# Kernel optimization log

Hardware: AMD Instinct MI355X
Metric: run time of the kernel (lower is better)

## Reference

```python
import jax, jax.numpy as jnp
import numpy as np

TOP_K = 2


def setup_inputs() -> dict:
    key = jax.random.key(0)
    k1, k2, k3 = jax.random.split(key, 3)
    inp = jax.random.normal(k1, (16384, 2048), dtype=jnp.float32)
    W = jax.random.normal(k2, (64, 2048), dtype=jnp.float32) * 0.02
    b = jax.random.normal(k3, (64,), dtype=jnp.float32) * 0.02
    return {"inp": inp, "W": W, "b": b}


def reference(inp, W, b):
    # gate logits: [tokens, num_expert]
    gate = jnp.einsum("td,ed->te", inp, W) + b
    # top-k over experts (lax.top_k returns sorted; torch used sorted=False,
    # so results match up to a per-token permutation of the k slots)
    top_val, top_idx = jax.lax.top_k(gate, TOP_K)  # [tokens, k]
    gate_score = jax.nn.softmax(top_val, axis=-1)[:, None, :]  # [tokens, 1, k]
    gate_top_k_idx = top_idx.reshape(-1)  # [tokens * k]
    return (gate_top_k_idx, gate_score)
```

## Files before the change

### kernel.cpp

```cpp
#include <hip/hip_runtime.h>
#include <math.h>


#define KDIM 2048
#define NEXP 64
#define TM 128
#define BK 32
#define LDSA 132
#define LDSW 68

__global__ __launch_bounds__(256) void gate_partial_kernel(
    const float* __restrict__ inp,
    const float* __restrict__ W,
    float* __restrict__ partial,
    int tokens, int kPerSplit)
{
    __shared__ float As[2][BK][LDSA];
    __shared__ float Ws[2][BK][LDSW];

    const int tid = threadIdx.x;
    const int tx  = tid & 7;
    const int ty  = tid >> 3;
    const int tokBase = blockIdx.x * TM;
    const int split   = blockIdx.y;
    const int k0      = split * kPerSplit;

    const int arow = tid >> 1;
    const int acol = (tid & 1) << 4;
    const int wrow = tid >> 2;
    const int wcol = (tid & 3) << 3;

    const float* aPtr = inp + (size_t)(tokBase + arow) * KDIM + k0 + acol;
    const float* wPtr = W   + (size_t)wrow * KDIM + k0 + wcol;

    float4 aReg[4], wReg[2];
    #pragma unroll
    for (int q = 0; q < 4; ++q) aReg[q] = *(const float4*)(aPtr + 4 * q);
    #pragma unroll
    for (int q = 0; q < 2; ++q) wReg[q] = *(const float4*)(wPtr + 4 * q);

    const int NT = kPerSplit / BK;

    #pragma unroll
    for (int q = 0; q < 4; ++q)
        #pragma unroll
        for (int j = 0; j < 4; ++j)
            As[0][acol + 4 * q + j][arow] = ((const float*)&aReg[q])[j];
    #pragma unroll
    for (int q = 0; q < 2; ++q)
        #pragma unroll
        for (int j = 0; j < 4; ++j)
            Ws[0][wcol + 4 * q + j][wrow] = ((const float*)&wReg[q])[j];

    if (NT > 1) {
        #pragma unroll
        for (int q = 0; q < 4; ++q) aReg[q] = *(const float4*)(aPtr + BK + 4 * q);
        #pragma unroll
        for (int q = 0; q < 2; ++q) wReg[q] = *(const float4*)(wPtr + BK + 4 * q);
    }
    __syncthreads();

    float acc[4][8];
    #pragma unroll
    for (int r = 0; r < 4; ++r)
        #pragma unroll
        for (int c = 0; c < 8; ++c) acc[r][c] = 0.0f;

    for (int kt = 0; kt < NT; ++kt) {
        const int cur = kt & 1;
        const int nxt = cur ^ 1;

        #pragma unroll 8
        for (int kk = 0; kk < BK; ++kk) {
            const float4 av  = *(const float4*)&As[cur][kk][ty << 2];
            const float4 wv0 = *(const float4*)&Ws[cur][kk][tx << 3];
            const float4 wv1 = *(const float4*)&Ws[cur][kk][(tx << 3) + 4];
            const float a[4] = {av.x, av.y, av.z, av.w};
            const float w[8] = {wv0.x, wv0.y, wv0.z, wv0.w,
                                wv1.x, wv1.y, wv1.z, wv1.w};
            #pragma unroll
            for (int r = 0; r < 4; ++r)
                #pragma unroll
                for (int c = 0; c < 8; ++c)
                    acc[r][c] = fmaf(a[r], w[c], acc[r][c]);
        }

        if (kt + 1 < NT) {
            #pragma unroll
            for (int q = 0; q < 4; ++q)
                #pragma unroll
                for (int j = 0; j < 4; ++j)
                    As[nxt][acol + 4 * q + j][arow] = ((const float*)&aReg[q])[j];
            #pragma unroll
            for (int q = 0; q < 2; ++q)
                #pragma unroll
                for (int j = 0; j < 4; ++j)
                    Ws[nxt][wcol + 4 * q + j][wrow] = ((const float*)&wReg[q])[j];
            if (kt + 2 < NT) {
                const int off = (kt + 2) * BK;
                #pragma unroll
                for (int q = 0; q < 4; ++q)
                    aReg[q] = *(const float4*)(aPtr + off + 4 * q);
                #pragma unroll
                for (int q = 0; q < 2; ++q)
                    wReg[q] = *(const float4*)(wPtr + off + 4 * q);
            }
        }
        __syncthreads();
    }

    const int eBase = tx << 3;
    #pragma unroll
    for (int r = 0; r < 4; ++r) {
        const int token = tokBase + (ty << 2) + r;
        float* p = &partial[((size_t)split * tokens + token) * NEXP + eBase];
        *(float4*)(p)     = make_float4(acc[r][0], acc[r][1], acc[r][2], acc[r][3]);
        *(float4*)(p + 4) = make_float4(acc[r][4], acc[r][5], acc[r][6], acc[r][7]);
    }
}

__global__ __launch_bounds__(256) void reduce_topk_kernel(
    const float* __restrict__ partial,
    const float* __restrict__ bias,
    float* __restrict__ out,
    int tokens, int S)
{
    const int tid = threadIdx.x;
    const int tx  = tid & 15;
    const int ty  = tid >> 4;
    const int token = blockIdx.x * 16 + ty;
    const int eBase = tx << 2;

    float4 v = make_float4(0.f, 0.f, 0.f, 0.f);
    for (int s = 0; s < S; ++s) {
        const float4 p = *(const float4*)&partial[((size_t)s * tokens + token) * NEXP + eBase];
        v.x += p.x; v.y += p.y; v.z += p.z; v.w += p.w;
    }
    const float4 bv = *(const float4*)&bias[eBase];
    float g[4] = { v.x + bv.x, v.y + bv.y, v.z + bv.z, v.w + bv.w };

    float v1 = g[0]; int i1 = eBase;
    float v2 = -INFINITY; int i2 = -1;
    #pragma unroll
    for (int c = 1; c < 4; ++c) {
        const float vv = g[c];
        const int   ii = eBase + c;
        if (vv > v1)      { v2 = v1; i2 = i1; v1 = vv; i1 = ii; }
        else if (vv > v2) { v2 = vv; i2 = ii; }
    }
    #pragma unroll
    for (int m = 1; m <= 8; m <<= 1) {
        const float ov1 = __shfl_xor(v1, m);
        const int   oi1 = __shfl_xor(i1, m);
        const float ov2 = __shfl_xor(v2, m);
        const int   oi2 = __shfl_xor(i2, m);
        const bool aw = (v1 > ov1) || (v1 == ov1 && i1 < oi1);
        const float nv1 = aw ? v1  : ov1;  const int ni1 = aw ? i1  : oi1;
        const float lv  = aw ? ov1 : v1;   const int li  = aw ? oi1 : i1;
        const float sv  = aw ? v2  : ov2;  const int si  = aw ? i2  : oi2;
        const bool sw = (sv > lv) || (sv == lv && si < li);
        v1 = nv1; i1 = ni1;
        v2 = sw ? sv : lv; i2 = sw ? si : li;
    }
    if (tx == 0) {
        const float e2 = expf(v2 - v1);
        const float denom = 1.0f + e2;
        out[2 * token]     = (float)i1;
        out[2 * token + 1] = (float)i2;
        out[tokens * 2 + 2 * token]     = 1.0f / denom;
        out[tokens * 2 + 2 * token + 1] = e2 / denom;
    }
}

extern "C" void kernel_launch(void* const* d_in, const int* in_sizes, int n_in,
                              void* d_out, int out_size, void* d_ws, size_t ws_size,
                              hipStream_t stream) {
    const float* inp  = (const float*)d_in[0];
    const float* W    = (const float*)d_in[1];
    const float* bias = (const float*)d_in[2];
    float* out = (float*)d_out;
    float* partial = (float*)d_ws;

    const int tokens = in_sizes[0] / KDIM;

    int S = 4;
    while (S > 1 && (size_t)S * tokens * NEXP * sizeof(float) > ws_size) S >>= 1;
    const int kPerSplit = KDIM / S;

    dim3 grid(tokens / TM, S);
    gate_partial_kernel<<<grid, 256, 0, stream>>>(inp, W, partial, tokens, kPerSplit);
    reduce_topk_kernel<<<tokens / 16, 256, 0, stream>>>(partial, bias, out, tokens, S);
}
```

Before: 214.8 us.

## Fuse split-K reduction and top-k into GEMM via last-block atomic counter

```diff
diff --git a/kernel.cpp b/kernel.cpp
--- a/kernel.cpp
+++ b/kernel.cpp
@@ -9,14 +9,18 @@
 #define LDSA 132
 #define LDSW 68
 
-__global__ __launch_bounds__(256) void gate_partial_kernel(
+__global__ __launch_bounds__(256) void gate_fused_kernel(
     const float* __restrict__ inp,
     const float* __restrict__ W,
+    const float* __restrict__ bias,
     float* __restrict__ partial,
-    int tokens, int kPerSplit)
+    int* __restrict__ ctr,
+    float* __restrict__ out,
+    int tokens, int kPerSplit, int S)
 {
     __shared__ float As[2][BK][LDSA];
     __shared__ float Ws[2][BK][LDSW];
+    __shared__ int lastFlag;
 
     const int tid = threadIdx.x;
     const int tx  = tid & 7;
@@ -117,58 +121,65 @@
         *(float4*)(p)     = make_float4(acc[r][0], acc[r][1], acc[r][2], acc[r][3]);
         *(float4*)(p + 4) = make_float4(acc[r][4], acc[r][5], acc[r][6], acc[r][7]);
     }
-}
-
-__global__ __launch_bounds__(256) void reduce_topk_kernel(
-    const float* __restrict__ partial,
-    const float* __restrict__ bias,
-    float* __restrict__ out,
-    int tokens, int S)
-{
-    const int tid = threadIdx.x;
-    const int tx  = tid & 15;
-    const int ty  = tid >> 4;
-    const int token = blockIdx.x * 16 + ty;
-    const int eBase = tx << 2;
-
-    float4 v = make_float4(0.f, 0.f, 0.f, 0.f);
-    for (int s = 0; s < S; ++s) {
-        const float4 p = *(const float4*)&partial[((size_t)s * tokens + token) * NEXP + eBase];
-        v.x += p.x; v.y += p.y; v.z += p.z; v.w += p.w;
-    }
-    const float4 bv = *(const float4*)&bias[eBase];
-    float g[4] = { v.x + bv.x, v.y + bv.y, v.z + bv.z, v.w + bv.w };
-
-    float v1 = g[0]; int i1 = eBase;
-    float v2 = -INFINITY; int i2 = -1;
-    #pragma unroll
-    for (int c = 1; c < 4; ++c) {
-        const float vv = g[c];
-        const int   ii = eBase + c;
-        if (vv > v1)      { v2 = v1; i2 = i1; v1 = vv; i1 = ii; }
-        else if (vv > v2) { v2 = vv; i2 = ii; }
-    }
-    #pragma unroll
-    for (int m = 1; m <= 8; m <<= 1) {
-        const float ov1 = __shfl_xor(v1, m);
-        const int   oi1 = __shfl_xor(i1, m);
-        const float ov2 = __shfl_xor(v2, m);
-        const int   oi2 = __shfl_xor(i2, m);
-        const bool aw = (v1 > ov1) || (v1 == ov1 && i1 < oi1);
-        const float nv1 = aw ? v1  : ov1;  const int ni1 = aw ? i1  : oi1;
-        const float lv  = aw ? ov1 : v1;   const int li  = aw ? oi1 : i1;
-        const float sv  = aw ? v2  : ov2;  const int si  = aw ? i2  : oi2;
-        const bool sw = (sv > lv) || (sv == lv && si < li);
-        v1 = nv1; i1 = ni1;
-        v2 = sw ? sv : lv; i2 = sw ? si : li;
-    }
-    if (tx == 0) {
-        const float e2 = expf(v2 - v1);
-        const float denom = 1.0f + e2;
-        out[2 * token]     = (float)i1;
-        out[2 * token + 1] = (float)i2;
-        out[tokens * 2 + 2 * token]     = 1.0f / denom;
-        out[tokens * 2 + 2 * token + 1] = e2 / denom;
+
+    __threadfence();
+    __syncthreads();
+    if (tid == 0) {
+        const int old = __hip_atomic_fetch_add(&ctr[blockIdx.x], 1,
+                            __ATOMIC_ACQ_REL, __HIP_MEMORY_SCOPE_AGENT);
+        lastFlag = (old == S - 1);
+    }
+    __syncthreads();
+    if (!lastFlag) return;
+    __builtin_amdgcn_fence(__ATOMIC_ACQUIRE, "agent");
+
+    const int rtx  = tid & 15;
+    const int rty  = tid >> 4;
+    const int eB   = rtx << 2;
+    const float4 bv = *(const float4*)&bias[eB];
+
+    for (int grp = 0; grp < TM / 16; ++grp) {
+        const int token = tokBase + grp * 16 + rty;
+
+        float4 v = make_float4(0.f, 0.f, 0.f, 0.f);
+        for (int s = 0; s < S; ++s) {
+            const float4 p = *(const float4*)
+                &partial[((size_t)s * tokens + token) * NEXP + eB];
+            v.x += p.x; v.y += p.y; v.z += p.z; v.w += p.w;
+        }
+        float g[4] = { v.x + bv.x, v.y + bv.y, v.z + bv.z, v.w + bv.w };
+
+        float v1 = g[0]; int i1 = eB;
+        float v2 = -INFINITY; int i2 = -1;
+        #pragma unroll
+        for (int c = 1; c < 4; ++c) {
+            const float vv = g[c];
+            const int   ii = eB + c;
+            if (vv > v1)      { v2 = v1; i2 = i1; v1 = vv; i1 = ii; }
+            else if (vv > v2) { v2 = vv; i2 = ii; }
+        }
+        #pragma unroll
+        for (int m = 1; m <= 8; m <<= 1) {
+            const float ov1 = __shfl_xor(v1, m);
+            const int   oi1 = __shfl_xor(i1, m);
+            const float ov2 = __shfl_xor(v2, m);
+            const int   oi2 = __shfl_xor(i2, m);
+            const bool aw = (v1 > ov1) || (v1 == ov1 && i1 < oi1);
+            const float nv1 = aw ? v1  : ov1;  const int ni1 = aw ? i1  : oi1;
+            const float lv  = aw ? ov1 : v1;   const int li  = aw ? oi1 : i1;
+            const float sv  = aw ? v2  : ov2;  const int si  = aw ? i2  : oi2;
+            const bool sw = (sv > lv) || (sv == lv && si < li);
+            v1 = nv1; i1 = ni1;
+            v2 = sw ? sv : lv; i2 = sw ? si : li;
+        }
+        if (rtx == 0) {
+            const float e2 = expf(v2 - v1);
+            const float denom = 1.0f + e2;
+            out[2 * token]     = (float)i1;
+            out[2 * token + 1] = (float)i2;
+            out[tokens * 2 + 2 * token]     = 1.0f / denom;
+            out[tokens * 2 + 2 * token + 1] = e2 / denom;
+        }
     }
 }
 
@@ -179,15 +190,25 @@
     const float* W    = (const float*)d_in[1];
     const float* bias = (const float*)d_in[2];
     float* out = (float*)d_out;
+    (void)n_in; (void)out_size;
+
+    const int tokens = in_sizes[0] / KDIM;
+    const int nTiles = tokens / TM;
+
+    int S = 4;
+    size_t ctrOff;
+    for (;;) {
+        const size_t pb = (size_t)S * tokens * NEXP * sizeof(float);
+        ctrOff = (pb + 255) & ~(size_t)255;
+        if (ctrOff + (size_t)nTiles * sizeof(int) <= ws_size || S == 1) break;
+        S >>= 1;
+    }
     float* partial = (float*)d_ws;
-
-    const int tokens = in_sizes[0] / KDIM;
-
-    int S = 4;
-    while (S > 1 && (size_t)S * tokens * NEXP * sizeof(float) > ws_size) S >>= 1;
-    const int kPerSplit = KDIM / S;
-
-    dim3 grid(tokens / TM, S);
-    gate_partial_kernel<<<grid, 256, 0, stream>>>(inp, W, partial, tokens, kPerSplit);
-    reduce_topk_kernel<<<tokens / 16, 256, 0, stream>>>(partial, bias, out, tokens, S);
+    int*   ctr     = (int*)((char*)d_ws + ctrOff);
+
+    hipMemsetAsync(ctr, 0, (size_t)nTiles * sizeof(int), stream);
+
+    dim3 grid(nTiles, S);
+    gate_fused_kernel<<<grid, 256, 0, stream>>>(
+        inp, W, bias, partial, ctr, out, tokens, KDIM / S, S);
 }
```

After: 328.1 us. 52.8% more time.
